# Optimization experiments

Hardware: AMD Instinct MI355X
Metric: run time of the kernel (lower is better)

## Reference

```python
import jax, jax.numpy as jnp
import numpy as np

N = 100000   # nodes
E = 1600000  # edges
IN = 128
HID = 128
OUT = 64
H = 4
DH = HID // H  # 32
EPS = 1e-5


def gatconv(x, W, al, ar, b, src, dst, heads, dh, act):
    """DGL GATConv: fc -> edge attn (leaky_relu 0.2) -> segment softmax over dst -> scatter sum -> bias -> act."""
    feat = (x @ W).reshape(-1, heads, dh)            # [N,H,dh]
    el = (feat * al).sum(-1)                          # [N,H]
    er = (feat * ar).sum(-1)                          # [N,H]
    e = jax.nn.leaky_relu(el[src] + er[dst], 0.2)     # [E,H]
    m = jax.ops.segment_max(e, dst, num_segments=N)   # [N,H]
    ex = jnp.exp(e - m[dst])                          # [E,H]
    s = jax.ops.segment_sum(ex, dst, num_segments=N)  # [N,H]
    alpha = ex / s[dst]                               # [E,H]
    msg = alpha[:, :, None] * feat[src]               # [E,H,dh]
    out = jax.ops.segment_sum(msg, dst, num_segments=N)  # [N,H,dh]
    out = out + b.reshape(1, heads, dh)
    return act(out) if act is not None else out


def layernorm(x, g, beta):
    mu = x.mean(-1, keepdims=True)
    var = ((x - mu) ** 2).mean(-1, keepdims=True)
    return (x - mu) * jax.lax.rsqrt(var + EPS) * g + beta


def setup_inputs():
    key = jax.random.key(0)
    ks = jax.random.split(key, 24)
    rn = lambda k, shape, s=0.05: jax.random.normal(k, shape, dtype=jnp.float32) * s
    return {
        "x": jax.random.normal(ks[0], (N, IN), dtype=jnp.float32),
        "src": jax.random.randint(ks[1], (E,), 0, N, dtype=jnp.int32),
        "dst": jax.random.randint(ks[2], (E,), 0, N, dtype=jnp.int32),
        "W0": rn(ks[3], (IN, H * DH)), "al0": rn(ks[4], (H, DH)), "ar0": rn(ks[5], (H, DH)), "b0": jnp.zeros((H * DH,), jnp.float32),
        "W1": rn(ks[6], (HID, H * DH)), "al1": rn(ks[7], (H, DH)), "ar1": rn(ks[8], (H, DH)), "b1": jnp.zeros((H * DH,), jnp.float32),
        "W2": rn(ks[9], (HID, HID)), "al2": rn(ks[10], (1, HID)), "ar2": rn(ks[11], (1, HID)), "b2": jnp.zeros((HID,), jnp.float32),
        "g0": jnp.ones((HID,), jnp.float32), "be0": jnp.zeros((HID,), jnp.float32),
        "g1": jnp.ones((HID,), jnp.float32), "be1": jnp.zeros((HID,), jnp.float32),
        "Wc": rn(ks[12], (HID, OUT)), "bc": jnp.zeros((OUT,), jnp.float32),
    }


def reference(x, src, dst, W0, al0, ar0, b0, W1, al1, ar1, b1, W2, al2, ar2, b2,
              g0, be0, g1, be1, Wc, bc):
    # layer 0 (heads=4, elu) -> flatten -> residual -> LN (dropout in eval = identity)
    h_res = x
    h = gatconv(x, W0, al0, ar0, b0, src, dst, H, DH, jax.nn.elu).reshape(N, HID)
    h = layernorm(h + h_res, g0, be0)
    # layer 1 (heads=4, elu)
    h_res = h
    h = gatconv(h, W1, al1, ar1, b1, src, dst, H, DH, jax.nn.elu).reshape(N, HID)
    h = layernorm(h + h_res, g1, be1)
    # layer 2 (heads=1, no activation) -> squeeze -> residual, no norm
    h_res = h
    h = gatconv(h, W2, al2, ar2, b2, src, dst, 1, HID, None).reshape(N, HID)
    h = h + h_res
    embedding = h
    logits = embedding @ Wc + bc
    return (logits, embedding)
```

## Files before the change

### kernel.cpp

```cpp
#include <hip/hip_runtime.h>

#define NN 100000
#define EE 1600000
#define BSHIFT 9
#define NBKT ((NN + 511) / 512)
#define CAP 10240
#define CHUNK 2048
#define NBLKA ((EE + CHUNK - 1) / CHUNK)

typedef float f32x4 __attribute__((ext_vector_type(4)));
typedef float f32x2 __attribute__((ext_vector_type(2)));
typedef short s16x8 __attribute__((ext_vector_type(8)));

__device__ __forceinline__ ushort f2bf(float x) {
  uint u = __float_as_uint(x);
  return (ushort)((u + 0x7fffu + ((u >> 16) & 1u)) >> 16);
}
__device__ __forceinline__ uint pack2bf(float x, float y) {
  return (uint)f2bf(x) | ((uint)f2bf(y) << 16);
}
__device__ __forceinline__ float bflo(uint p) { return __uint_as_float(p << 16); }
__device__ __forceinline__ float bfhi(uint p) { return __uint_as_float(p & 0xffff0000u); }

__global__ __launch_bounds__(256) void k_prep(const float* __restrict__ W0,
    const float* __restrict__ al0, const float* __restrict__ ar0,
    const float* __restrict__ W1, const float* __restrict__ al1, const float* __restrict__ ar1,
    const float* __restrict__ W2, const float* __restrict__ al2, const float* __restrict__ ar2,
    float* __restrict__ waug) {
  int t = threadIdx.x;
  for (int o = t; o < 3 * 1024; o += 256) {
    int L = o >> 10, rem = o & 1023, c = rem >> 7, k = rem & 127;
    const float* W = (L == 0) ? W0 : (L == 1) ? W1 : W2;
    float v = 0.f;
    if (L < 2) {
      int h = c & 3;
      const float* a = (c < 4) ? ((L == 0) ? al0 : al1) : ((L == 0) ? ar0 : ar1);
      for (int d = 0; d < 32; ++d) v += W[k * 128 + h * 32 + d] * a[h * 32 + d];
    } else {
      if (c == 0)      { for (int j = 0; j < 128; ++j) v += W[k * 128 + j] * al2[j]; }
      else if (c == 1) { for (int j = 0; j < 128; ++j) v += W[k * 128 + j] * ar2[j]; }
    }
    waug[o] = v;
  }
}

template<int M, bool ABF, int ELER>
__global__ __launch_bounds__(256) void gemm_mfma(const void* __restrict__ Av,
    const float* __restrict__ W, const float* __restrict__ bias,
    float* __restrict__ outf, ushort* __restrict__ feat8s,
    const float* __restrict__ waug,
    float* __restrict__ el, float* __restrict__ er, int N) {
  constexpr int MT = (ELER > 0) ? 144 : M;
  constexpr int NT = MT / 16;
  __shared__ ushort Wt[MT * 136];
  const int tid = threadIdx.x;
  for (int idx = tid; idx < 128 * M; idx += 256) {
    int k = idx / M, c = idx - k * M;
    Wt[c * 136 + k] = f2bf(W[idx]);
  }
  if (ELER > 0) {
    for (int idx = tid; idx < 8 * 128; idx += 256) {
      int c = idx >> 7, k = idx & 127;
      Wt[(128 + c) * 136 + k] = f2bf(waug[idx]);
      Wt[(136 + c) * 136 + k] = 0;
    }
  }
  __syncthreads();
  const int wid = tid >> 6, lane = tid & 63;
  const int rl = lane & 15, grp = lane >> 4;
  const long row0 = (long)blockIdx.x * 128;

  s16x8 af[2][4];
#pragma unroll
  for (int rt = 0; rt < 2; ++rt) {
    long row = row0 + rt * 64 + wid * 16 + rl;
    if (row >= N) row = N - 1;
    if (ABF) {
      const s16x8* Ar = (const s16x8*)((const ushort*)Av + row * 128);
#pragma unroll
      for (int ks = 0; ks < 4; ++ks) af[rt][ks] = Ar[ks * 4 + grp];
    } else {
      const float4* Ar = (const float4*)((const float*)Av + row * 128);
#pragma unroll
      for (int ks = 0; ks < 4; ++ks) {
        float4 a0 = Ar[ks * 8 + grp * 2];
        float4 a1 = Ar[ks * 8 + grp * 2 + 1];
        s16x8 f;
        f[0] = (short)f2bf(a0.x); f[1] = (short)f2bf(a0.y);
        f[2] = (short)f2bf(a0.z); f[3] = (short)f2bf(a0.w);
        f[4] = (short)f2bf(a1.x); f[5] = (short)f2bf(a1.y);
        f[6] = (short)f2bf(a1.z); f[7] = (short)f2bf(a1.w);
        af[rt][ks] = f;
      }
    }
  }
  f32x4 acc[2][NT];
#pragma unroll
  for (int rt = 0; rt < 2; ++rt)
#pragma unroll
    for (int ct = 0; ct < NT; ++ct) acc[rt][ct] = (f32x4)(0.f);

#pragma unroll
  for (int ct = 0; ct < NT; ++ct) {
#pragma unroll
    for (int ks = 0; ks < 4; ++ks) {
      s16x8 bf = *(const s16x8*)&Wt[(ct * 16 + rl) * 136 + ks * 32 + grp * 8];
      acc[0][ct] = __builtin_amdgcn_mfma_f32_16x16x32_bf16(af[0][ks], bf, acc[0][ct], 0, 0, 0);
      acc[1][ct] = __builtin_amdgcn_mfma_f32_16x16x32_bf16(af[1][ks], bf, acc[1][ct], 0, 0, 0);
    }
  }

  if (ELER > 0) __syncthreads();

#pragma unroll
  for (int rt = 0; rt < 2; ++rt) {
#pragma unroll
    for (int ct = 0; ct < NT; ++ct) {
      int col = ct * 16 + rl;
      float bb = (ELER == 0) ? bias[col] : 0.f;
#pragma unroll
      for (int j = 0; j < 4; ++j) {
        int lrow = rt * 64 + wid * 16 + grp * 4 + j;
        long grow = row0 + lrow;
        if (ELER > 0) {
          if (ct < 8) {
            Wt[lrow * 128 + col] = f2bf(acc[rt][ct][j]);
          } else if (rl < 8 && grow < N) {
            float v = acc[rt][ct][j];
            if (ELER == 4) {
              if (rl < 4) el[grow * 4 + rl] = v;
              else        er[grow * 4 + (rl - 4)] = v;
            } else {
              if (rl == 0)      el[grow] = v;
              else if (rl == 1) er[grow] = v;
            }
          }
        } else if (grow < N) {
          outf[grow * M + col] = acc[rt][ct][j] + bb;
        }
      }
    }
  }

  if (ELER > 0) {
    __syncthreads();
    const uint* stage = (const uint*)Wt;
    const int rhalf = lane >> 5, ei = lane & 31;
    uint* f8u = (uint*)feat8s;
#pragma unroll 4
    for (int rr = 0; rr < 16; ++rr) {
      int lrow = wid * 32 + rr * 2 + rhalf;
      long grow = row0 + lrow;
      uint2 pq = *(const uint2*)&stage[lrow * 64 + ei * 2];
      int u = __builtin_amdgcn_cvt_pk_fp8_f32(bflo(pq.x), bfhi(pq.x), 0, false);
      u = __builtin_amdgcn_cvt_pk_fp8_f32(bflo(pq.y), bfhi(pq.y), u, true);
      if (grow < N) f8u[grow * 32 + ei] = (uint)u;
    }
  }
}

__global__ __launch_bounds__(256) void k_partA(const int* __restrict__ src,
    const int* __restrict__ dst, uint* __restrict__ bcnt, uint* __restrict__ tmp) {
  __shared__ uint hist[NBKT], excl[NBKT], gbase[NBKT], cur[NBKT];
  __shared__ uint2 recs[CHUNK];
  const int t = threadIdx.x;
  const long e0 = (long)blockIdx.x * CHUNK;
  const int cnt = (EE - e0 < CHUNK) ? (int)(EE - e0) : CHUNK;
  for (int i = t; i < NBKT; i += 256) hist[i] = 0;
  __syncthreads();
  for (int i = t; i < cnt; i += 256) {
    int d = dst[e0 + i];
    atomicAdd(&hist[d >> BSHIFT], 1u);
  }
  __syncthreads();
  if (t == 0) {
    uint run = 0;
    for (int i = 0; i < NBKT; ++i) { excl[i] = run; run += hist[i]; }
  }
  __syncthreads();
  if (t < NBKT) {
    gbase[t] = atomicAdd(&bcnt[t], hist[t]);
    cur[t] = excl[t];
  }
  __syncthreads();
  for (int i = t; i < cnt; i += 256) {
    uint s = (uint)src[e0 + i], d = (uint)dst[e0 + i];
    uint p = atomicAdd(&cur[d >> BSHIFT], 1u);
    recs[p] = make_uint2(s, d);
  }
  __syncthreads();
  for (int i = t; i < cnt; i += 256) {
    uint2 r = recs[i];
    uint b = r.y >> BSHIFT;
    uint pos = gbase[b] + ((uint)i - excl[b]);
    if (pos < CAP) tmp[(long)b * CAP + pos] = r.x | ((r.y & 511u) << 17);
  }
}

__global__ __launch_bounds__(256) void k_bscan(const uint* __restrict__ bcnt,
    uint* __restrict__ bbase, int* __restrict__ indptr) {
  __shared__ uint lds[NBKT];
  int t = threadIdx.x;
  if (t < NBKT) lds[t] = bcnt[t];
  __syncthreads();
  if (t == 0) {
    uint run = 0;
    for (int i = 0; i < NBKT; ++i) { bbase[i] = run; run += lds[i]; }
    indptr[NN] = (int)run;
  }
}

__global__ __launch_bounds__(256) void k_partB(const uint* __restrict__ bcnt,
    const uint* __restrict__ bbase, const uint* __restrict__ tmp,
    int* __restrict__ indptr, int* __restrict__ ssrc) {
  __shared__ uint hist[512], cur[512], wsum[256];
  __shared__ uint stage[CAP];
  const int b = blockIdx.x, t = threadIdx.x;
  const int dlo = b << BSHIFT;
  const int nn = (NN - dlo < 512) ? (NN - dlo) : 512;
  int nrec = (int)bcnt[b];
  if (nrec > CAP) nrec = CAP;
  const uint base = bbase[b];
  const uint* tb = tmp + (long)b * CAP;
  for (int i = t; i < 512; i += 256) hist[i] = 0;
  __syncthreads();
  for (int i = t; i < nrec; i += 256) {
    atomicAdd(&hist[tb[i] >> 17], 1u);
  }
  __syncthreads();
  uint a0 = hist[t * 2], a1 = hist[t * 2 + 1];
  uint ts = a0 + a1;
  wsum[t] = ts;
  __syncthreads();
  for (int st = 1; st < 256; st <<= 1) {
    uint v = (t >= st) ? wsum[t - st] : 0;
    __syncthreads();
    wsum[t] += v;
    __syncthreads();
  }
  uint texcl = wsum[t] - ts;
  cur[t * 2] = texcl;
  cur[t * 2 + 1] = texcl + a0;
  if (t * 2 < nn)     indptr[dlo + t * 2]     = (int)(base + texcl);
  if (t * 2 + 1 < nn) indptr[dlo + t * 2 + 1] = (int)(base + texcl + a0);
  __syncthreads();
  for (int i = t; i < nrec; i += 256) {
    uint v = tb[i];
    uint rel = atomicAdd(&cur[v >> 17], 1u);
    stage[rel] = v & 0x1FFFFu;
  }
  __syncthreads();
  for (int i = t; i < nrec; i += 256) {
    ssrc[base + i] = (int)stage[i];
  }
}

template<int HEADS, bool FINAL, bool PREVBF>
__global__ __launch_bounds__(256) void gat_aggregate(
    const int* __restrict__ indptr, const int* __restrict__ ssrc,
    const char* __restrict__ el8, const float* __restrict__ er,
    const char* __restrict__ feat8, const float* __restrict__ bias,
    const void* __restrict__ prevv, const float* __restrict__ g,
    const float* __restrict__ beta, void* __restrict__ outv,
    ushort* __restrict__ embb, int N) {
  int wave = threadIdx.x >> 6, lane = threadIdx.x & 63;
  long n = (long)blockIdx.x * 4 + wave;
  if (n >= N) return;
  const int b = __builtin_amdgcn_readfirstlane(indptr[n]);
  const int e = __builtin_amdgcn_readfirstlane(indptr[n + 1]);
  const int deg = e - b;
  const int l5 = lane & 31, half = lane >> 5;
  const int head = (HEADS == 4) ? (l5 >> 3) : 0;
  const float er0 = (HEADS == 4) ? er[n * 4 + head] : er[n];
  const int* sp = ssrc + b;
  const uint lpart = (uint)l5 * 4u;
  const uint hoff = (uint)head * 4u;

  float a0 = 0.f, a1 = 0.f, a2 = 0.f, a3 = 0.f, s = 0.f;
  const int npair = (deg + 1) >> 1;
  for (int p = 0; p < npair; p += 4) {
#pragma unroll
    for (int k = 0; k < 4; ++k) {
      const int pk = p + k;
      int ja = 2 * pk;     if (ja > deg - 1) ja = deg - 1;
      int jb = 2 * pk + 1; if (jb > deg - 1) jb = deg - 1;
      uint sna = (uint)sp[ja], snb = (uint)sp[jb];
      uint fo = ((half ? snb : sna) << 7) + lpart;
      uint v = *(const uint*)(feat8 + fo);
      float elv;
      if (HEADS == 4) elv = *(const float*)(el8 + (((half ? snb : sna) << 4) + hoff));
      else            elv = *(const float*)(el8 + ((half ? snb : sna) << 2));
      float ev = elv + er0;
      ev = fmaxf(ev, 0.f) + 0.2f * fminf(ev, 0.f);
      float w = __expf(ev);
      w = (2 * pk + half < deg) ? w : 0.f;
      auto f01 = __builtin_amdgcn_cvt_pk_f32_fp8((int)v, false);
      auto f23 = __builtin_amdgcn_cvt_pk_f32_fp8((int)v, true);
      s += w;
      a0 = fmaf(w, f01[0], a0);
      a1 = fmaf(w, f01[1], a1);
      a2 = fmaf(w, f23[0], a2);
      a3 = fmaf(w, f23[1], a3);
    }
  }
  a0 += __shfl_xor(a0, 32, 64);
  a1 += __shfl_xor(a1, 32, 64);
  a2 += __shfl_xor(a2, 32, 64);
  a3 += __shfl_xor(a3, 32, 64);
  s  += __shfl_xor(s, 32, 64);

  float inv = (s > 0.f) ? 1.f / s : 0.f;
  float v0 = a0 * inv, v1 = a1 * inv, v2 = a2 * inv, v3 = a3 * inv;
  float4 bb = ((const float4*)bias)[l5];
  v0 += bb.x; v1 += bb.y; v2 += bb.z; v3 += bb.w;
  if (!FINAL) {
    v0 = v0 > 0.f ? v0 : __expf(v0) - 1.f;
    v1 = v1 > 0.f ? v1 : __expf(v1) - 1.f;
    v2 = v2 > 0.f ? v2 : __expf(v2) - 1.f;
    v3 = v3 > 0.f ? v3 : __expf(v3) - 1.f;
  }
  if (PREVBF) {
    uint2 pp = ((const uint2*)prevv)[n * 32 + l5];
    v0 += bflo(pp.x); v1 += bfhi(pp.x);
    v2 += bflo(pp.y); v3 += bfhi(pp.y);
  } else {
    float4 ph = ((const float4*)prevv)[n * 32 + l5];
    v0 += ph.x; v1 += ph.y; v2 += ph.z; v3 += ph.w;
  }
  if (!FINAL) {
    float sum = v0 + v1 + v2 + v3;
#pragma unroll
    for (int m = 16; m; m >>= 1) sum += __shfl_xor(sum, m, 64);
    float mu = sum * (1.f / 128.f);
    float d0 = v0 - mu, d1 = v1 - mu, d2 = v2 - mu, d3 = v3 - mu;
    float vs = d0 * d0 + d1 * d1 + d2 * d2 + d3 * d3;
#pragma unroll
    for (int m = 16; m; m >>= 1) vs += __shfl_xor(vs, m, 64);
    float rstd = rsqrtf(vs * (1.f / 128.f) + 1e-5f);
    float4 g4 = ((const float4*)g)[l5];
    float4 be4 = ((const float4*)beta)[l5];
    float o0 = d0 * rstd * g4.x + be4.x;
    float o1 = d1 * rstd * g4.y + be4.y;
    float o2 = d2 * rstd * g4.z + be4.z;
    float o3 = d3 * rstd * g4.w + be4.w;
    if (!half) ((uint2*)outv)[n * 32 + l5] = make_uint2(pack2bf(o0, o1), pack2bf(o2, o3));
  } else {
    if (!half) {
      ((float4*)outv)[n * 32 + l5] = make_float4(v0, v1, v2, v3);
      ((uint2*)embb)[n * 32 + l5] = make_uint2(pack2bf(v0, v1), pack2bf(v2, v3));
    }
  }
}

extern "C" void kernel_launch(void* const* d_in, const int* in_sizes, int n_in,
                              void* d_out, int out_size, void* d_ws, size_t ws_size,
                              hipStream_t stream) {
  const float* x   = (const float*)d_in[0];
  const int*   src = (const int*)d_in[1];
  const int*   dst = (const int*)d_in[2];
  const float* W0  = (const float*)d_in[3];
  const float* al0 = (const float*)d_in[4];
  const float* ar0 = (const float*)d_in[5];
  const float* b0  = (const float*)d_in[6];
  const float* W1  = (const float*)d_in[7];
  const float* al1 = (const float*)d_in[8];
  const float* ar1 = (const float*)d_in[9];
  const float* b1  = (const float*)d_in[10];
  const float* W2  = (const float*)d_in[11];
  const float* al2 = (const float*)d_in[12];
  const float* ar2 = (const float*)d_in[13];
  const float* b2  = (const float*)d_in[14];
  const float* g0  = (const float*)d_in[15];
  const float* be0 = (const float*)d_in[16];
  const float* g1  = (const float*)d_in[17];
  const float* be1 = (const float*)d_in[18];
  const float* Wc  = (const float*)d_in[19];
  const float* bc  = (const float*)d_in[20];

  float* out    = (float*)d_out;
  float* logits = out;
  float* emb    = out + (long)NN * 64;

  char*   feat8 = (char*)d_ws;
  float*  el    = (float*)(feat8 + (size_t)NN * 128);
  float*  er    = el + (long)NN * 4;
  ushort* bufAb = (ushort*)(er + (long)NN * 4);
  ushort* bufBb = bufAb + (long)NN * 128;
  uint*   tmp   = (uint*)(bufBb + (long)NN * 128);
  uint*   bcnt  = tmp + (long)NBKT * CAP;
  uint*   bbase = bcnt + NBKT;
  float*  waug  = (float*)(bbase + NBKT);
  ushort* feat8s = (ushort*)feat8;
  char*   el8   = (char*)el;

  int* indptr = (int*)d_out;
  int* ssrc   = indptr + NN + 1;

  const int gN4 = (NN + 3) / 4;
  const int gGm = (NN + 127) / 128;

  k_prep<<<1, 256, 0, stream>>>(W0, al0, ar0, W1, al1, ar1, W2, al2, ar2, waug);
  hipMemsetAsync(bcnt, 0, NBKT * sizeof(uint), stream);
  k_partA<<<NBLKA, 256, 0, stream>>>(src, dst, bcnt, tmp);
  k_bscan<<<1, 256, 0, stream>>>(bcnt, bbase, indptr);
  k_partB<<<NBKT, 256, 0, stream>>>(bcnt, bbase, tmp, indptr, ssrc);

  gemm_mfma<128, false, 4><<<gGm, 256, 0, stream>>>(x, W0, nullptr, nullptr, feat8s, waug, el, er, NN);
  gat_aggregate<4, false, false><<<gN4, 256, 0, stream>>>(indptr, ssrc, el8, er, feat8, b0, x, g0, be0, bufAb, nullptr, NN);

  gemm_mfma<128, true, 4><<<gGm, 256, 0, stream>>>(bufAb, W1, nullptr, nullptr, feat8s, waug + 1024, el, er, NN);
  gat_aggregate<4, false, true><<<gN4, 256, 0, stream>>>(indptr, ssrc, el8, er, feat8, b1, bufAb, g1, be1, bufBb, nullptr, NN);

  gemm_mfma<128, true, 1><<<gGm, 256, 0, stream>>>(bufBb, W2, nullptr, nullptr, feat8s, waug + 2048, el, er, NN);
  gat_aggregate<1, true, true><<<gN4, 256, 0, stream>>>(indptr, ssrc, el8, er, feat8, b2, bufBb, nullptr, nullptr, emb, bufAb, NN);

  gemm_mfma<64, true, 0><<<gGm, 256, 0, stream>>>(bufAb, Wc, bc, logits, nullptr, nullptr, nullptr, nullptr, NN);
}
```

Baseline: 332.1 us.

## Fold prep and bucket scan into partition kernels, peel aggregate loop tail

Moves the weight-attention precompute into an extra block of the partition-A kernel, and has every partition-B block recompute the bucket prefix scan locally, removing two tiny single-block launches. indptr[NN] is set to the constant edge count. The aggregation loop now runs full groups of edge pairs without clamping or masking, with a separate masked tail loop for the remainder. These cut launch overhead and per-edge branch/select work, at the cost of redundant scans in each partition-B block and the assumption that no bucket overflows.

```diff
diff --git a/kernel.cpp b/kernel.cpp
--- a/kernel.cpp
+++ b/kernel.cpp
@@ -9,7 +9,6 @@
 #define NBLKA ((EE + CHUNK - 1) / CHUNK)
 
 typedef float f32x4 __attribute__((ext_vector_type(4)));
-typedef float f32x2 __attribute__((ext_vector_type(2)));
 typedef short s16x8 __attribute__((ext_vector_type(8)));
 
 __device__ __forceinline__ ushort f2bf(float x) {
@@ -21,28 +20,6 @@
 }
 __device__ __forceinline__ float bflo(uint p) { return __uint_as_float(p << 16); }
 __device__ __forceinline__ float bfhi(uint p) { return __uint_as_float(p & 0xffff0000u); }
-
-__global__ __launch_bounds__(256) void k_prep(const float* __restrict__ W0,
-    const float* __restrict__ al0, const float* __restrict__ ar0,
-    const float* __restrict__ W1, const float* __restrict__ al1, const float* __restrict__ ar1,
-    const float* __restrict__ W2, const float* __restrict__ al2, const float* __restrict__ ar2,
-    float* __restrict__ waug) {
-  int t = threadIdx.x;
-  for (int o = t; o < 3 * 1024; o += 256) {
-    int L = o >> 10, rem = o & 1023, c = rem >> 7, k = rem & 127;
-    const float* W = (L == 0) ? W0 : (L == 1) ? W1 : W2;
-    float v = 0.f;
-    if (L < 2) {
-      int h = c & 3;
-      const float* a = (c < 4) ? ((L == 0) ? al0 : al1) : ((L == 0) ? ar0 : ar1);
-      for (int d = 0; d < 32; ++d) v += W[k * 128 + h * 32 + d] * a[h * 32 + d];
-    } else {
-      if (c == 0)      { for (int j = 0; j < 128; ++j) v += W[k * 128 + j] * al2[j]; }
-      else if (c == 1) { for (int j = 0; j < 128; ++j) v += W[k * 128 + j] * ar2[j]; }
-    }
-    waug[o] = v;
-  }
-}
 
 template<int M, bool ABF, int ELER>
 __global__ __launch_bounds__(256) void gemm_mfma(const void* __restrict__ Av,
@@ -160,10 +137,31 @@
 }
 
 __global__ __launch_bounds__(256) void k_partA(const int* __restrict__ src,
-    const int* __restrict__ dst, uint* __restrict__ bcnt, uint* __restrict__ tmp) {
+    const int* __restrict__ dst, uint* __restrict__ bcnt, uint* __restrict__ tmp,
+    const float* __restrict__ W0, const float* __restrict__ al0, const float* __restrict__ ar0,
+    const float* __restrict__ W1, const float* __restrict__ al1, const float* __restrict__ ar1,
+    const float* __restrict__ W2, const float* __restrict__ al2, const float* __restrict__ ar2,
+    float* __restrict__ waug) {
+  const int t = threadIdx.x;
+  if (blockIdx.x == NBLKA) {
+    for (int o = t; o < 3 * 1024; o += 256) {
+      int L = o >> 10, rem = o & 1023, c = rem >> 7, k = rem & 127;
+      const float* W = (L == 0) ? W0 : (L == 1) ? W1 : W2;
+      float v = 0.f;
+      if (L < 2) {
+        int h = c & 3;
+        const float* a = (c < 4) ? ((L == 0) ? al0 : al1) : ((L == 0) ? ar0 : ar1);
+        for (int d = 0; d < 32; ++d) v += W[k * 128 + h * 32 + d] * a[h * 32 + d];
+      } else {
+        if (c == 0)      { for (int j = 0; j < 128; ++j) v += W[k * 128 + j] * al2[j]; }
+        else if (c == 1) { for (int j = 0; j < 128; ++j) v += W[k * 128 + j] * ar2[j]; }
+      }
+      waug[o] = v;
+    }
+    return;
+  }
   __shared__ uint hist[NBKT], excl[NBKT], gbase[NBKT], cur[NBKT];
   __shared__ uint2 recs[CHUNK];
-  const int t = threadIdx.x;
   const long e0 = (long)blockIdx.x * CHUNK;
   const int cnt = (EE - e0 < CHUNK) ? (int)(EE - e0) : CHUNK;
   for (int i = t; i < NBKT; i += 256) hist[i] = 0;
@@ -197,30 +195,26 @@
   }
 }
 
-__global__ __launch_bounds__(256) void k_bscan(const uint* __restrict__ bcnt,
-    uint* __restrict__ bbase, int* __restrict__ indptr) {
-  __shared__ uint lds[NBKT];
-  int t = threadIdx.x;
-  if (t < NBKT) lds[t] = bcnt[t];
-  __syncthreads();
-  if (t == 0) {
-    uint run = 0;
-    for (int i = 0; i < NBKT; ++i) { bbase[i] = run; run += lds[i]; }
-    indptr[NN] = (int)run;
-  }
-}
-
 __global__ __launch_bounds__(256) void k_partB(const uint* __restrict__ bcnt,
-    const uint* __restrict__ bbase, const uint* __restrict__ tmp,
-    int* __restrict__ indptr, int* __restrict__ ssrc) {
+    const uint* __restrict__ tmp, int* __restrict__ indptr, int* __restrict__ ssrc) {
   __shared__ uint hist[512], cur[512], wsum[256];
   __shared__ uint stage[CAP];
   const int b = blockIdx.x, t = threadIdx.x;
+  stage[t] = (t < NBKT) ? bcnt[t] : 0;
+  __syncthreads();
+  for (int st = 1; st < 256; st <<= 1) {
+    uint v = (t >= st) ? stage[t - st] : 0;
+    __syncthreads();
+    stage[t] += v;
+    __syncthreads();
+  }
+  const uint base = (b == 0) ? 0u : stage[b - 1];
+  if (b == 0 && t == 0) indptr[NN] = EE;
+  __syncthreads();
   const int dlo = b << BSHIFT;
   const int nn = (NN - dlo < 512) ? (NN - dlo) : 512;
   int nrec = (int)bcnt[b];
   if (nrec > CAP) nrec = CAP;
-  const uint base = bbase[b];
   const uint* tb = tmp + (long)b * CAP;
   for (int i = t; i < 512; i += 256) hist[i] = 0;
   __syncthreads();
@@ -277,23 +271,21 @@
   const uint hoff = (uint)head * 4u;
 
   float a0 = 0.f, a1 = 0.f, a2 = 0.f, a3 = 0.f, s = 0.f;
+  const int nfull = deg >> 1;
+  const int nmain = nfull & ~3;
   const int npair = (deg + 1) >> 1;
-  for (int p = 0; p < npair; p += 4) {
+  for (int p = 0; p < nmain; p += 4) {
 #pragma unroll
     for (int k = 0; k < 4; ++k) {
       const int pk = p + k;
-      int ja = 2 * pk;     if (ja > deg - 1) ja = deg - 1;
-      int jb = 2 * pk + 1; if (jb > deg - 1) jb = deg - 1;
-      uint sna = (uint)sp[ja], snb = (uint)sp[jb];
-      uint fo = ((half ? snb : sna) << 7) + lpart;
-      uint v = *(const uint*)(feat8 + fo);
-      float elv;
-      if (HEADS == 4) elv = *(const float*)(el8 + (((half ? snb : sna) << 4) + hoff));
-      else            elv = *(const float*)(el8 + ((half ? snb : sna) << 2));
+      uint sna = (uint)sp[2 * pk], snb = (uint)sp[2 * pk + 1];
+      uint sel = half ? snb : sna;
+      uint v = *(const uint*)(feat8 + ((sel << 7) + lpart));
+      float elv = (HEADS == 4) ? *(const float*)(el8 + ((sel << 4) + hoff))
+                               : *(const float*)(el8 + (sel << 2));
       float ev = elv + er0;
       ev = fmaxf(ev, 0.f) + 0.2f * fminf(ev, 0.f);
       float w = __expf(ev);
-      w = (2 * pk + half < deg) ? w : 0.f;
       auto f01 = __builtin_amdgcn_cvt_pk_f32_fp8((int)v, false);
       auto f23 = __builtin_amdgcn_cvt_pk_f32_fp8((int)v, true);
       s += w;
@@ -302,6 +294,25 @@
       a2 = fmaf(w, f23[0], a2);
       a3 = fmaf(w, f23[1], a3);
     }
+  }
+  for (int p = nmain; p < npair; ++p) {
+    int jb = 2 * p + 1; if (jb > deg - 1) jb = deg - 1;
+    uint sna = (uint)sp[2 * p], snb = (uint)sp[jb];
+    uint sel = half ? snb : sna;
+    uint v = *(const uint*)(feat8 + ((sel << 7) + lpart));
+    float elv = (HEADS == 4) ? *(const float*)(el8 + ((sel << 4) + hoff))
+                             : *(const float*)(el8 + (sel << 2));
+    float ev = elv + er0;
+    ev = fmaxf(ev, 0.f) + 0.2f * fminf(ev, 0.f);
+    float w = __expf(ev);
+    w = (2 * p + half < deg) ? w : 0.f;
+    auto f01 = __builtin_amdgcn_cvt_pk_f32_fp8((int)v, false);
+    auto f23 = __builtin_amdgcn_cvt_pk_f32_fp8((int)v, true);
+    s += w;
+    a0 = fmaf(w, f01[0], a0);
+    a1 = fmaf(w, f01[1], a1);
+    a2 = fmaf(w, f23[0], a2);
+    a3 = fmaf(w, f23[1], a3);
   }
   a0 += __shfl_xor(a0, 32, 64);
   a1 += __shfl_xor(a1, 32, 64);
@@ -388,8 +399,7 @@
   ushort* bufBb = bufAb + (long)NN * 128;
   uint*   tmp   = (uint*)(bufBb + (long)NN * 128);
   uint*   bcnt  = tmp + (long)NBKT * CAP;
-  uint*   bbase = bcnt + NBKT;
-  float*  waug  = (float*)(bbase + NBKT);
+  float*  waug  = (float*)(bcnt + NBKT);
   ushort* feat8s = (ushort*)feat8;
   char*   el8   = (char*)el;
 
@@ -399,11 +409,10 @@
   const int gN4 = (NN + 3) / 4;
   const int gGm = (NN + 127) / 128;
 
-  k_prep<<<1, 256, 0, stream>>>(W0, al0, ar0, W1, al1, ar1, W2, al2, ar2, waug);
   hipMemsetAsync(bcnt, 0, NBKT * sizeof(uint), stream);
-  k_partA<<<NBLKA, 256, 0, stream>>>(src, dst, bcnt, tmp);
-  k_bscan<<<1, 256, 0, stream>>>(bcnt, bbase, indptr);
-  k_partB<<<NBKT, 256, 0, stream>>>(bcnt, bbase, tmp, indptr, ssrc);
+  k_partA<<<NBLKA + 1, 256, 0, stream>>>(src, dst, bcnt, tmp,
+      W0, al0, ar0, W1, al1, ar1, W2, al2, ar2, waug);
+  k_partB<<<NBKT, 256, 0, stream>>>(bcnt, tmp, indptr, ssrc);
 
   gemm_mfma<128, false, 4><<<gGm, 256, 0, stream>>>(x, W0, nullptr, nullptr, feat8s, waug, el, er, NN);
   gat_aggregate<4, false, false><<<gN4, 256, 0, stream>>>(indptr, ssrc, el8, er, feat8, b0, x, g0, be0, bufAb, nullptr, NN);
```

Result: faster. 314.2 us (-5.4%).
